# Kernel optimization log

Hardware: AMD Instinct MI355X
Metric: run time of the kernel (lower is better)

## Reference

```python
import math
import jax, jax.numpy as jnp
import numpy as np

N_HEADS = 12


def _rel_to_abs(x):
    # x: [b, h, L, 2L-1] relative logits -> [b, h, L, L] absolute-position scores
    b, h, L, _ = x.shape
    x = jnp.pad(x, ((0, 0), (0, 0), (0, 0), (0, 1)))           # [b,h,L,2L]
    xf = x.reshape(b, h, L * 2 * L)
    xf = jnp.pad(xf, ((0, 0), (0, 0), (0, L - 1)))
    return xf.reshape(b, h, L + 1, 2 * L - 1)[:, :, :L, L - 1:]


def _abs_to_rel(x):
    # x: [b, h, L, L] attention weights -> [b, h, L, 2L-1] relative-position weights
    b, h, L, _ = x.shape
    x = jnp.pad(x, ((0, 0), (0, 0), (0, 0), (0, L - 1)))        # [b,h,L,2L-1]
    xf = x.reshape(b, h, L * (2 * L - 1))
    xf = jnp.pad(xf, ((0, 0), (0, 0), (L, 0)))
    return xf.reshape(b, h, L, 2 * L)[:, :, :, 1:]


def _get_relative_embeddings(emb, length):
    # emb: [n_rel, 2*window+1, k] -> [n_rel, 2*length-1, k]
    window = (emb.shape[1] - 1) // 2
    pad_len = max(length - (window + 1), 0)
    start = max(window + 1 - length, 0)
    if pad_len > 0:
        emb = jnp.pad(emb, ((0, 0), (pad_len, pad_len), (0, 0)))
    return emb[:, start:start + 2 * length - 1]


def setup_inputs() -> dict:
    key = jax.random.key(0)
    ks = jax.random.split(key, 8)
    B, C, T, H = 4, 768, 1024, N_HEADS
    K = C // H
    W = 10
    xavier = math.sqrt(2.0 / (C + C))          # xavier_uniform std analogue
    rel_std = K ** (-0.5)
    return {
        "x": jax.random.normal(ks[0], (B, C, T), jnp.float32),
        "c": jax.random.normal(ks[1], (B, C, T), jnp.float32),
        "Wq": jax.random.normal(ks[2], (C, C), jnp.float32) * xavier,
        "bq": jnp.zeros((C,), jnp.float32),
        "Wk": jax.random.normal(ks[3], (C, C), jnp.float32) * xavier,
        "bk": jnp.zeros((C,), jnp.float32),
        "Wv": jax.random.normal(ks[4], (C, C), jnp.float32) * xavier,
        "bv": jnp.zeros((C,), jnp.float32),
        "Wo": jax.random.normal(ks[5], (C, C), jnp.float32) * xavier,
        "bo": jnp.zeros((C,), jnp.float32),
        "emb_rel_k": jax.random.normal(ks[6], (1, 2 * W + 1, K), jnp.float32) * rel_std,
        "emb_rel_v": jax.random.normal(ks[7], (1, 2 * W + 1, K), jnp.float32) * rel_std,
    }


def reference(x, c, Wq, bq, Wk, bk, Wv, bv, Wo, bo, emb_rel_k, emb_rel_v):
    B, C, T = x.shape
    H = N_HEADS
    K = C // H

    def proj(W_, b_, inp):  # Conv1d(kernel=1) == channel-wise linear
        return jnp.einsum('oi,bit->bot', W_, inp) + b_[None, :, None]

    # [B,C,T] -> [B,H,T,K]
    q = proj(Wq, bq, x).reshape(B, H, K, T).transpose(0, 1, 3, 2)
    k = proj(Wk, bk, c).reshape(B, H, K, T).transpose(0, 1, 3, 2)
    v = proj(Wv, bv, c).reshape(B, H, K, T).transpose(0, 1, 3, 2)

    qs = q * (1.0 / math.sqrt(K))
    scores = jnp.einsum('bhtd,bhsd->bhts', qs, k)               # [B,H,T,T]

    # relative key logits via skewing trick
    rel_k = _get_relative_embeddings(emb_rel_k, T)              # [1,2T-1,K]
    rel_logits = jnp.einsum('bhtd,md->bhtm', qs, rel_k[0])      # [B,H,T,2T-1]
    scores = scores + _rel_to_abs(rel_logits)

    # proximal bias: -log(1 + |i - j|)
    r = jnp.arange(T, dtype=scores.dtype)
    scores = scores - jnp.log1p(jnp.abs(r[None, :] - r[:, None]))[None, None]

    p = jax.nn.softmax(scores, axis=-1)
    out = jnp.einsum('bhts,bhsd->bhtd', p, v)                   # [B,H,T,K]

    # relative value contribution
    rel_v = _get_relative_embeddings(emb_rel_v, T)              # [1,2T-1,K]
    out = out + jnp.einsum('bhtm,md->bhtd', _abs_to_rel(p), rel_v[0])

    out = out.transpose(0, 1, 3, 2).reshape(B, C, T)            # [B,C,T]
    return jnp.einsum('oi,bit->bot', Wo, out) + bo[None, :, None]
```

## Files before the change

kernel.cpp:

```cpp
#include <hip/hip_runtime.h>
#include <hip/hip_bf16.h>

using bf16 = __hip_bfloat16;
typedef __attribute__((ext_vector_type(8))) short short8;
typedef __attribute__((ext_vector_type(4))) float f32x4;

static constexpr int C = 768, T = 1024, H = 12, D = 64;

__device__ __forceinline__ f32x4 mfma16(short8 a, short8 b, f32x4 c){
  return __builtin_amdgcn_mfma_f32_16x16x32_bf16(a, b, c, 0, 0, 0);
}

__device__ __forceinline__ void gload16(const void* g, void* l){
  void* gv = const_cast<void*>(g);
  __builtin_amdgcn_global_load_lds((__attribute__((address_space(1))) void*)gv,
                                   (__attribute__((address_space(3))) void*)l, 16, 0, 0);
}

__device__ __forceinline__ float b2f(short s){
  unsigned u = ((unsigned)(unsigned short)s) << 16;
  return __builtin_bit_cast(float, u);
}

__device__ __forceinline__ int cvtpk(float a, float b){
  int r;
  asm("v_cvt_pk_bf16_f32 %0, %1, %2" : "=v"(r) : "v"(a), "v"(b));
  return r;
}

union PkU { int i[4]; short8 v; };

__global__ __launch_bounds__(256) void cvt4_kernel(const float* __restrict__ a,
                                                   const float* __restrict__ b,
                                                   const float* __restrict__ c_,
                                                   const float* __restrict__ d,
                                                   bf16* oa, bf16* ob, bf16* oc, bf16* od){
  const int m = blockIdx.y;
  const float* in = m==0 ? a : m==1 ? b : m==2 ? c_ : d;
  bf16* out = m==0 ? oa : m==1 ? ob : m==2 ? oc : od;
  int i = (blockIdx.x*256 + threadIdx.x)*4;
  float4 v = *(const float4*)(in + i);
  out[i+0] = (bf16)v.x; out[i+1] = (bf16)v.y;
  out[i+2] = (bf16)v.z; out[i+3] = (bf16)v.w;
}

__global__ __launch_bounds__(256) void transpose_cvt2(const float* __restrict__ xin,
                                                      const float* __restrict__ cin,
                                                      bf16* __restrict__ xo,
                                                      bf16* __restrict__ co){
  __shared__ float tile[64][65];
  const int z = blockIdx.z, b = z & 3, which = z >> 2;
  const float* in = which ? cin : xin;
  bf16* out = which ? co : xo;
  const int t0 = blockIdx.x*64, c0 = blockIdx.y*64;
  const int u = threadIdx.x & 63, r0 = threadIdx.x >> 6;
  const float* ip = in + ((size_t)b*C + c0)*T + t0;
  #pragma unroll
  for (int i = r0; i < 64; i += 4) tile[i][u] = ip[(size_t)i*T + u];
  __syncthreads();
  bf16* op = out + ((size_t)b*T + t0)*C + c0;
  #pragma unroll
  for (int j = r0; j < 64; j += 4) op[(size_t)j*C + u] = (bf16)tile[u][j];
}

__global__ __launch_bounds__(256,3) void gemm_qkv(const bf16* __restrict__ xb,
    const bf16* __restrict__ cb, const bf16* __restrict__ wq, const bf16* __restrict__ wk,
    const bf16* __restrict__ wv, const float* __restrict__ bq, const float* __restrict__ bk,
    const float* __restrict__ bv, bf16* __restrict__ qout, bf16* __restrict__ kout,
    bf16* __restrict__ vout){
  const int tid = threadIdx.x, lane = tid & 63, w = tid >> 6;
  const int wr = w >> 1, wc = w & 1, g = lane >> 4, cl = lane & 15;
  const int bz = blockIdx.y, b = bz & 3, mode = bz >> 2;
  const int lb = blockIdx.x;
  int m0, n0;
  if (mode == 2){ m0 = (lb >> 3)*128; n0 = (lb & 7)*128; }
  else          { m0 = (lb / 6)*128;  n0 = (lb % 6)*128; }
  const bf16* A  = (mode==0) ? xb + (size_t)b*T*C : (mode==1) ? cb + (size_t)b*T*C : wv;
  const bf16* Bp = (mode==2) ? cb + (size_t)b*T*C : (mode==0) ? wq : wk;
  const float* bias = (mode==0) ? bq : (mode==1) ? bk : bv;
  const float scale = (mode==0) ? 0.125f*1.44269504088896f : 1.0f;
  __shared__ bf16 lA[128*64], lB[128*64];
  f32x4 acc[4][4] = {};
  const bf16* Ars = A  + (size_t)m0*768;
  const bf16* Brs = Bp + (size_t)n0*768;
  for (int k0 = 0; k0 < 768; k0 += 64){
    __syncthreads();
    #pragma unroll
    for (int rr = 0; rr < 4; ++rr){
      const int u = rr*256 + tid;
      const int row = u >> 3, cc = u & 7;
      const int src = row*768 + k0 + ((cc ^ (row & 7))*8);
      gload16(Ars + src, &lA[(size_t)u*8]);
      gload16(Brs + src, &lB[(size_t)u*8]);
    }
    __syncthreads();
    #pragma unroll
    for (int kh = 0; kh < 2; ++kh){
      short8 af[4], bfr[4];
      #pragma unroll
      for (int mi = 0; mi < 4; ++mi){
        const int row = wr*64 + mi*16 + cl;
        af[mi] = *(const short8*)&lA[row*64 + (((g + kh*4) ^ (row & 7))*8)];
      }
      #pragma unroll
      for (int ni = 0; ni < 4; ++ni){
        const int row = wc*64 + ni*16 + cl;
        bfr[ni] = *(const short8*)&lB[row*64 + (((g + kh*4) ^ (row & 7))*8)];
      }
      __builtin_amdgcn_s_setprio(1);
      #pragma unroll
      for (int mi = 0; mi < 4; ++mi)
        #pragma unroll
        for (int ni = 0; ni < 4; ++ni)
          acc[mi][ni] = mfma16(af[mi], bfr[ni], acc[mi][ni]);
      __builtin_amdgcn_s_setprio(0);
    }
  }
  #pragma unroll
  for (int mi = 0; mi < 4; ++mi){
    const int mB = m0 + wr*64 + mi*16 + g*4;
    #pragma unroll
    for (int ni = 0; ni < 4; ++ni){
      const int n = n0 + wc*64 + ni*16 + cl;
      #pragma unroll
      for (int r = 0; r < 4; ++r){
        const int m = mB + r;
        float v = acc[mi][ni][r];
        if (mode <= 1){
          v = (v + bias[n]) * scale;
          bf16* outp = mode ? kout : qout;
          outp[(size_t)b*(H*T*D) + (size_t)(n >> 6)*(T*D) + (size_t)m*D + (n & 63)] = (bf16)v;
        } else {
          v += bias[m];
          vout[(size_t)b*(C*T) + (size_t)m*T + n] = (bf16)v;
        }
      }
    }
  }
}

__global__ __launch_bounds__(256,3) void gemm_o(const bf16* __restrict__ wo,
                                                const bf16* __restrict__ attn,
                                                const float* __restrict__ bias,
                                                float* __restrict__ outp){
  const int tid = threadIdx.x, lane = tid & 63, w = tid >> 6;
  const int wr = w >> 1, wc = w & 1, g = lane >> 4, cl = lane & 15;
  const int b = blockIdx.z;
  const int m0 = blockIdx.x*128, n0 = blockIdx.y*128;
  __shared__ bf16 lA[128*64], lB[128*64];
  f32x4 acc[4][4] = {};
  const bf16* Ars = wo + (size_t)m0*768;
  const bf16* Brs = attn + (size_t)b*T*C + (size_t)n0*768;
  for (int k0 = 0; k0 < 768; k0 += 64){
    __syncthreads();
    #pragma unroll
    for (int rr = 0; rr < 4; ++rr){
      const int u = rr*256 + tid;
      const int row = u >> 3, cc = u & 7;
      const int src = row*768 + k0 + ((cc ^ (row & 7))*8);
      gload16(Ars + src, &lA[(size_t)u*8]);
      gload16(Brs + src, &lB[(size_t)u*8]);
    }
    __syncthreads();
    #pragma unroll
    for (int kh = 0; kh < 2; ++kh){
      short8 af[4], bfr[4];
      #pragma unroll
      for (int mi = 0; mi < 4; ++mi){
        const int row = wr*64 + mi*16 + cl;
        af[mi] = *(const short8*)&lA[row*64 + (((g + kh*4) ^ (row & 7))*8)];
      }
      #pragma unroll
      for (int ni = 0; ni < 4; ++ni){
        const int row = wc*64 + ni*16 + cl;
        bfr[ni] = *(const short8*)&lB[row*64 + (((g + kh*4) ^ (row & 7))*8)];
      }
      __builtin_amdgcn_s_setprio(1);
      #pragma unroll
      for (int mi = 0; mi < 4; ++mi)
        #pragma unroll
        for (int ni = 0; ni < 4; ++ni)
          acc[mi][ni] = mfma16(af[mi], bfr[ni], acc[mi][ni]);
      __builtin_amdgcn_s_setprio(0);
    }
  }
  #pragma unroll
  for (int mi = 0; mi < 4; ++mi){
    const int mB = m0 + wr*64 + mi*16 + g*4;
    #pragma unroll
    for (int ni = 0; ni < 4; ++ni){
      const int n = n0 + wc*64 + ni*16 + cl;
      #pragma unroll
      for (int r = 0; r < 4; ++r){
        const int m = mB + r;
        outp[(size_t)b*(C*T) + (size_t)m*T + n] = acc[mi][ni][r] + bias[m];
      }
    }
  }
}

__global__ __launch_bounds__(256,3) void attn_kernel(const bf16* __restrict__ qws,
                                                     const bf16* __restrict__ kws,
                                                     const bf16* __restrict__ vws,
                                                     bf16* __restrict__ aws,
                                                     const float* __restrict__ relk,
                                                     const float* __restrict__ relv){
  const int tid = threadIdx.x, lane = tid & 63, w = tid >> 6;
  const int g = lane >> 4, cl = lane & 15;
  const int i0 = blockIdx.x*64, bh = blockIdx.y;
  const int b = bh / H, h = bh % H;
  const int ql = w*16 + cl;
  const int qt = i0 + ql;

  __shared__ __align__(16) char smem[40960];
  bf16*  lKV   = (bf16*)smem;
  float* bandS = (float*)(smem + 32768);
  bf16*  relkD = (bf16*)(smem + 38144);
  bf16*  lEmb32 = lKV + 4096;
  bf16*  lEV    = lKV;
  bf16*  lQ     = lKV + 3*4096;

  const bf16* qg = qws + ((size_t)bh*T + i0)*D;
  const bf16* kg = kws + (size_t)bh*T*D;
  const bf16* vg = vws + ((size_t)b*C + h*D)*T;

  int kOff[2], vOff[2], qOff[2], dst[2];
  #pragma unroll
  for (int r = 0; r < 2; ++r){
    const int u = r*256 + tid, L = u >> 3, cc = u & 7;
    const int sc8 = (cc ^ (L & 7))*8;
    const int sig = (((L>>4)&1)<<5) | (((L>>2)&3)<<3) | (((L>>5)&1)<<2) | (L&3);
    kOff[r] = sig*64 + sc8;
    vOff[r] = L*T + sc8;
    qOff[r] = L*64 + sc8;
    dst[r]  = u*8;
  }

  #pragma unroll
  for (int r = 0; r < 2; ++r){
    gload16(qg + qOff[r], &lQ[dst[r]]);
    gload16(kg + kOff[r], &lKV[dst[r]]);
    gload16(vg + vOff[r], &lKV[2*4096 + dst[r]]);
  }
  for (int idx = tid; idx < 2048; idx += 256){
    const int row = idx >> 6, col = idx & 63;
    const float v = (row < 21) ? relk[idx] : 0.0f;
    lEmb32[row*64 + (((col >> 3) ^ (row & 7))*8) + (col & 7)] = (bf16)v;
  }
  __syncthreads();

  const short8 aq0 = *(const short8*)&lQ[ql*64 + ((g ^ (ql & 7))*8)];
  const short8 aq1 = *(const short8*)&lQ[ql*64 + (((g + 4) ^ (ql & 7))*8)];

  #pragma unroll
  for (int ni2 = 0; ni2 < 2; ++ni2){
    const int row = ni2*16 + cl;
    short8 e0 = *(const short8*)&lEmb32[row*64 + ((g ^ (row & 7))*8)];
    short8 e1 = *(const short8*)&lEmb32[row*64 + (((g + 4) ^ (row & 7))*8)];
    f32x4 rk = {};
    rk = mfma16(e0, aq0, rk);
    rk = mfma16(e1, aq1, rk);
    #pragma unroll
    for (int rr = 0; rr < 4; ++rr){
      const int ridx = ni2*16 + 4*g + rr;
      if (ridx < 21) relkD[ql*22 + ridx] = (bf16)rk[rr];
    }
  }
  __syncthreads();

  float mreg = -1e30f, lreg = 0.f;
  f32x4 o[4] = {};
  const int koffA[4] = {8*g, 32 + 8*g, 4 + 8*g, 36 + 8*g};

  for (int jt = 0; jt < 16; ++jt){
    const int j0 = jt*64, cur = jt & 1, nxt = cur ^ 1;
    if (jt < 15){
      const int jn = j0 + 64;
      #pragma unroll
      for (int r = 0; r < 2; ++r){
        gload16(kg + jn*64 + kOff[r], &lKV[nxt*4096 + dst[r]]);
        gload16(vg + jn + vOff[r],    &lKV[(2 + nxt)*4096 + dst[r]]);
      }
    }
    const bf16* Kc = lKV + cur*4096;
    const bf16* Vc = lKV + (2 + cur)*4096;

    f32x4 s[4] = {};
    __builtin_amdgcn_s_setprio(1);
    #pragma unroll
    for (int ni = 0; ni < 4; ++ni){
      const int row = ni*16 + cl;
      short8 k0f = *(const short8*)&Kc[row*64 + ((g ^ (row & 7))*8)];
      s[ni] = mfma16(k0f, aq0, s[ni]);
      short8 k1f = *(const short8*)&Kc[row*64 + (((g + 4) ^ (row & 7))*8)];
      s[ni] = mfma16(k1f, aq1, s[ni]);
    }
    __builtin_amdgcn_s_setprio(0);

    const int dj = j0 - i0;
    if (dj == 0 || dj == 64 || dj == -64){
      #pragma unroll
      for (int ni = 0; ni < 4; ++ni){
        const int ibase = j0 + koffA[ni] - qt;
        #pragma unroll
        for (int r = 0; r < 4; ++r){
          const int dd = ibase + r;
          float v = s[ni][r] - __log2f(fabsf((float)dd) + 1.0f);
          if ((unsigned)(dd + 10) <= 20u){
            v += b2f(*(const short*)&relkD[ql*22 + dd + 10]);
            bandS[ql*21 + dd + 10] = v;
          }
          s[ni][r] = v;
        }
      }
    } else {
      #pragma unroll
      for (int ni = 0; ni < 4; ++ni){
        const float fb = (float)(j0 + koffA[ni] - qt);
        #pragma unroll
        for (int r = 0; r < 4; ++r)
          s[ni][r] -= __log2f(fabsf(fb + (float)r) + 1.0f);
      }
    }

    float m0 = fmaxf(fmaxf(s[0][0], s[0][1]), fmaxf(s[0][2], s[0][3]));
    float m1 = fmaxf(fmaxf(s[1][0], s[1][1]), fmaxf(s[1][2], s[1][3]));
    float m2 = fmaxf(fmaxf(s[2][0], s[2][1]), fmaxf(s[2][2], s[2][3]));
    float m3 = fmaxf(fmaxf(s[3][0], s[3][1]), fmaxf(s[3][2], s[3][3]));
    float mx = fmaxf(fmaxf(m0, m1), fmaxf(m2, m3));
    mx = fmaxf(mx, __shfl_xor(mx, 16));
    mx = fmaxf(mx, __shfl_xor(mx, 32));
    const float mn = fmaxf(mreg, mx);
    if (!__all(mn == mreg)){
      const float sc = __builtin_amdgcn_exp2f(mreg - mn);
      lreg *= sc;
      #pragma unroll
      for (int di = 0; di < 4; ++di)
        #pragma unroll
        for (int r = 0; r < 4; ++r) o[di][r] *= sc;
      mreg = mn;
    }
    float rs = 0.f;
    #pragma unroll
    for (int ni = 0; ni < 4; ++ni)
      #pragma unroll
      for (int r = 0; r < 4; ++r){
        float p = __builtin_amdgcn_exp2f(s[ni][r] - mreg);
        s[ni][r] = p; rs += p;
      }
    rs += __shfl_xor(rs, 16);
    rs += __shfl_xor(rs, 32);
    lreg += rs;

    PkU bf0, bf1;
    bf0.i[0] = cvtpk(s[0][0], s[0][1]); bf0.i[1] = cvtpk(s[0][2], s[0][3]);
    bf0.i[2] = cvtpk(s[2][0], s[2][1]); bf0.i[3] = cvtpk(s[2][2], s[2][3]);
    bf1.i[0] = cvtpk(s[1][0], s[1][1]); bf1.i[1] = cvtpk(s[1][2], s[1][3]);
    bf1.i[2] = cvtpk(s[3][0], s[3][1]); bf1.i[3] = cvtpk(s[3][2], s[3][3]);

    __builtin_amdgcn_s_setprio(1);
    #pragma unroll
    for (int di = 0; di < 4; ++di){
      const int vrow = di*16 + cl;
      short8 a0 = *(const short8*)&Vc[vrow*64 + ((g ^ (vrow & 7))*8)];
      o[di] = mfma16(a0, bf0.v, o[di]);
      short8 a1 = *(const short8*)&Vc[vrow*64 + (((g + 4) ^ (vrow & 7))*8)];
      o[di] = mfma16(a1, bf1.v, o[di]);
    }
    __builtin_amdgcn_s_setprio(0);
    __syncthreads();
  }

  for (int idx = tid; idx < 2048; idx += 256){
    const int d = idx >> 5, c = idx & 31;
    const float v = (c < 21) ? relv[c*64 + d] : 0.0f;
    lEV[d*32 + (((c >> 3) ^ ((d >> 2) & 3))*8) + (c & 7)] = (bf16)v;
  }
  __syncthreads();

  const float invl = 1.0f / lreg;
  float pb[8];
  #pragma unroll
  for (int e = 0; e < 8; ++e){
    const int ddi = 8*g + e;
    float pv = 0.f;
    if (ddi < 21){
      const int j = qt + ddi - 10;
      if (j >= 0 && j < T)
        pv = __builtin_amdgcn_exp2f(bandS[ql*21 + ddi] - mreg) * invl;
    }
    pb[e] = pv;
  }
  PkU bfE;
  bfE.i[0] = cvtpk(pb[0], pb[1]); bfE.i[1] = cvtpk(pb[2], pb[3]);
  bfE.i[2] = cvtpk(pb[4], pb[5]); bfE.i[3] = cvtpk(pb[6], pb[7]);

  bf16* outp = aws + (size_t)(b*T + qt)*C + h*64;
  #pragma unroll
  for (int di = 0; di < 4; ++di){
    const int arow = di*16 + cl;
    short8 aE = *(const short8*)&lEV[arow*32 + ((g ^ ((arow >> 2) & 3))*8)];
    f32x4 z = {};
    f32x4 ba = mfma16(aE, bfE.v, z);
    const int p0 = cvtpk(o[di][0]*invl + ba[0], o[di][1]*invl + ba[1]);
    const int p1 = cvtpk(o[di][2]*invl + ba[2], o[di][3]*invl + ba[3]);
    *(int2*)(outp + di*16 + 4*g) = make_int2(p0, p1);
  }
}

extern "C" void kernel_launch(void* const* d_in, const int* in_sizes, int n_in,
                              void* d_out, int out_size, void* d_ws, size_t ws_size,
                              hipStream_t stream){
  const float* x    = (const float*)d_in[0];
  const float* cin  = (const float*)d_in[1];
  const float* Wq   = (const float*)d_in[2];
  const float* bq   = (const float*)d_in[3];
  const float* Wk   = (const float*)d_in[4];
  const float* bk   = (const float*)d_in[5];
  const float* Wv   = (const float*)d_in[6];
  const float* bv   = (const float*)d_in[7];
  const float* Wo   = (const float*)d_in[8];
  const float* bo   = (const float*)d_in[9];
  const float* relk = (const float*)d_in[10];
  const float* relv = (const float*)d_in[11];

  char* ws = (char*)d_ws;
  constexpr size_t SZ_W = (size_t)768*768*2;
  constexpr size_t SZ_T = (size_t)4*1024*768*2;
  bf16* wq  = (bf16*)(ws + 0*SZ_W);
  bf16* wk  = (bf16*)(ws + 1*SZ_W);
  bf16* wv  = (bf16*)(ws + 2*SZ_W);
  bf16* wo  = (bf16*)(ws + 3*SZ_W);
  bf16* xb  = (bf16*)(ws + 4*SZ_W);
  bf16* cb  = (bf16*)(ws + 4*SZ_W + 1*SZ_T);
  bf16* qws = (bf16*)(ws + 4*SZ_W + 2*SZ_T);
  bf16* kws = (bf16*)(ws + 4*SZ_W + 3*SZ_T);
  bf16* vws = (bf16*)(ws + 4*SZ_W + 4*SZ_T);
  bf16* attn = xb;

  cvt4_kernel<<<dim3(576,4), 256, 0, stream>>>(Wq, Wk, Wv, Wo, wq, wk, wv, wo);
  transpose_cvt2<<<dim3(16,12,8), 256, 0, stream>>>(x, cin, xb, cb);
  gemm_qkv<<<dim3(48,12), 256, 0, stream>>>(xb, cb, wq, wk, wv, bq, bk, bv, qws, kws, vws);
  attn_kernel<<<dim3(16,48), 256, 0, stream>>>(qws, kws, vws, attn, relk, relv);
  gemm_o<<<dim3(6,8,4), 256, 0, stream>>>(wo, attn, bo, (float*)d_out);
}
```

Measured before the change: 100.7 us.

## Merge prep kernels, load V fragments directly to registers in attention

```diff
diff --git a/kernel.cpp b/kernel.cpp
--- a/kernel.cpp
+++ b/kernel.cpp
@@ -30,37 +30,37 @@
 
 union PkU { int i[4]; short8 v; };
 
-__global__ __launch_bounds__(256) void cvt4_kernel(const float* __restrict__ a,
-                                                   const float* __restrict__ b,
-                                                   const float* __restrict__ c_,
-                                                   const float* __restrict__ d,
-                                                   bf16* oa, bf16* ob, bf16* oc, bf16* od){
-  const int m = blockIdx.y;
-  const float* in = m==0 ? a : m==1 ? b : m==2 ? c_ : d;
-  bf16* out = m==0 ? oa : m==1 ? ob : m==2 ? oc : od;
-  int i = (blockIdx.x*256 + threadIdx.x)*4;
-  float4 v = *(const float4*)(in + i);
-  out[i+0] = (bf16)v.x; out[i+1] = (bf16)v.y;
-  out[i+2] = (bf16)v.z; out[i+3] = (bf16)v.w;
-}
-
-__global__ __launch_bounds__(256) void transpose_cvt2(const float* __restrict__ xin,
-                                                      const float* __restrict__ cin,
-                                                      bf16* __restrict__ xo,
-                                                      bf16* __restrict__ co){
-  __shared__ float tile[64][65];
-  const int z = blockIdx.z, b = z & 3, which = z >> 2;
-  const float* in = which ? cin : xin;
-  bf16* out = which ? co : xo;
-  const int t0 = blockIdx.x*64, c0 = blockIdx.y*64;
-  const int u = threadIdx.x & 63, r0 = threadIdx.x >> 6;
-  const float* ip = in + ((size_t)b*C + c0)*T + t0;
-  #pragma unroll
-  for (int i = r0; i < 64; i += 4) tile[i][u] = ip[(size_t)i*T + u];
-  __syncthreads();
-  bf16* op = out + ((size_t)b*T + t0)*C + c0;
-  #pragma unroll
-  for (int j = r0; j < 64; j += 4) op[(size_t)j*C + u] = (bf16)tile[u][j];
+__global__ __launch_bounds__(256) void prep_kernel(const float* __restrict__ xin,
+    const float* __restrict__ cin, const float* __restrict__ Wq,
+    const float* __restrict__ Wk, const float* __restrict__ Wv,
+    const float* __restrict__ Wo, bf16* __restrict__ xo, bf16* __restrict__ co,
+    bf16* __restrict__ wq, bf16* __restrict__ wk, bf16* __restrict__ wv,
+    bf16* __restrict__ wo){
+  const int z = blockIdx.z;
+  if (z < 8){
+    __shared__ float tile[64][65];
+    const int b = z & 3, which = z >> 2;
+    const float* in = which ? cin : xin;
+    bf16* out = which ? co : xo;
+    const int t0 = blockIdx.x*64, c0 = blockIdx.y*64;
+    const int u = threadIdx.x & 63, r0 = threadIdx.x >> 6;
+    const float* ip = in + ((size_t)b*C + c0)*T + t0;
+    #pragma unroll
+    for (int i = r0; i < 64; i += 4) tile[i][u] = ip[(size_t)i*T + u];
+    __syncthreads();
+    bf16* op = out + ((size_t)b*T + t0)*C + c0;
+    #pragma unroll
+    for (int j = r0; j < 64; j += 4) op[(size_t)j*C + u] = (bf16)tile[u][j];
+  } else {
+    const int chunk = (z - 8)*192 + blockIdx.y*16 + blockIdx.x;
+    const int m = chunk / 576;
+    const int off = (chunk % 576)*1024 + threadIdx.x*4;
+    const float* in = m==0 ? Wq : m==1 ? Wk : m==2 ? Wv : Wo;
+    bf16* out = m==0 ? wq : m==1 ? wk : m==2 ? wv : wo;
+    float4 v = *(const float4*)(in + off);
+    out[off+0] = (bf16)v.x; out[off+1] = (bf16)v.y;
+    out[off+2] = (bf16)v.z; out[off+3] = (bf16)v.w;
+  }
 }
 
 __global__ __launch_bounds__(256,3) void gemm_qkv(const bf16* __restrict__ xb,
@@ -199,7 +199,7 @@
   }
 }
 
-__global__ __launch_bounds__(256,3) void attn_kernel(const bf16* __restrict__ qws,
+__global__ __launch_bounds__(256,5) void attn_kernel(const bf16* __restrict__ qws,
                                                      const bf16* __restrict__ kws,
                                                      const bf16* __restrict__ vws,
                                                      bf16* __restrict__ aws,
@@ -212,26 +212,25 @@
   const int ql = w*16 + cl;
   const int qt = i0 + ql;
 
-  __shared__ __align__(16) char smem[40960];
-  bf16*  lKV   = (bf16*)smem;
-  float* bandS = (float*)(smem + 32768);
-  bf16*  relkD = (bf16*)(smem + 38144);
-  bf16*  lEmb32 = lKV + 4096;
-  bf16*  lEV    = lKV;
-  bf16*  lQ     = lKV + 3*4096;
+  __shared__ __align__(16) char smem[24576];
+  bf16*  lK     = (bf16*)smem;
+  float* bandS  = (float*)(smem + 16384);
+  bf16*  relkD  = (bf16*)(smem + 21760);
+  bf16*  lEmb32 = (bf16*)(smem + 16384);
+  bf16*  lEV    = (bf16*)smem;
+  bf16*  lQ     = lK + 4096;
 
   const bf16* qg = qws + ((size_t)bh*T + i0)*D;
   const bf16* kg = kws + (size_t)bh*T*D;
   const bf16* vg = vws + ((size_t)b*C + h*D)*T;
 
-  int kOff[2], vOff[2], qOff[2], dst[2];
+  int kOff[2], qOff[2], dst[2];
   #pragma unroll
   for (int r = 0; r < 2; ++r){
     const int u = r*256 + tid, L = u >> 3, cc = u & 7;
     const int sc8 = (cc ^ (L & 7))*8;
     const int sig = (((L>>4)&1)<<5) | (((L>>2)&3)<<3) | (((L>>5)&1)<<2) | (L&3);
     kOff[r] = sig*64 + sc8;
-    vOff[r] = L*T + sc8;
     qOff[r] = L*64 + sc8;
     dst[r]  = u*8;
   }
@@ -239,8 +238,7 @@
   #pragma unroll
   for (int r = 0; r < 2; ++r){
     gload16(qg + qOff[r], &lQ[dst[r]]);
-    gload16(kg + kOff[r], &lKV[dst[r]]);
-    gload16(vg + vOff[r], &lKV[2*4096 + dst[r]]);
+    gload16(kg + kOff[r], &lK[dst[r]]);
   }
   for (int idx = tid; idx < 2048; idx += 256){
     const int row = idx >> 6, col = idx & 63;
@@ -274,16 +272,22 @@
 
   for (int jt = 0; jt < 16; ++jt){
     const int j0 = jt*64, cur = jt & 1, nxt = cur ^ 1;
+
+    short8 va[8];
+    #pragma unroll
+    for (int di = 0; di < 4; ++di){
+      const bf16* p = vg + (size_t)(di*16 + cl)*T + j0 + 8*g;
+      va[di*2 + 0] = *(const short8*)(p);
+      va[di*2 + 1] = *(const short8*)(p + 32);
+    }
+
     if (jt < 15){
       const int jn = j0 + 64;
       #pragma unroll
-      for (int r = 0; r < 2; ++r){
-        gload16(kg + jn*64 + kOff[r], &lKV[nxt*4096 + dst[r]]);
-        gload16(vg + jn + vOff[r],    &lKV[(2 + nxt)*4096 + dst[r]]);
-      }
-    }
-    const bf16* Kc = lKV + cur*4096;
-    const bf16* Vc = lKV + (2 + cur)*4096;
+      for (int r = 0; r < 2; ++r)
+        gload16(kg + jn*64 + kOff[r], &lK[nxt*4096 + dst[r]]);
+    }
+    const bf16* Kc = lK + cur*4096;
 
     f32x4 s[4] = {};
     __builtin_amdgcn_s_setprio(1);
@@ -361,11 +365,8 @@
     __builtin_amdgcn_s_setprio(1);
     #pragma unroll
     for (int di = 0; di < 4; ++di){
-      const int vrow = di*16 + cl;
-      short8 a0 = *(const short8*)&Vc[vrow*64 + ((g ^ (vrow & 7))*8)];
-      o[di] = mfma16(a0, bf0.v, o[di]);
-      short8 a1 = *(const short8*)&Vc[vrow*64 + (((g + 4) ^ (vrow & 7))*8)];
-      o[di] = mfma16(a1, bf1.v, o[di]);
+      o[di] = mfma16(va[di*2 + 0], bf0.v, o[di]);
+      o[di] = mfma16(va[di*2 + 1], bf1.v, o[di]);
     }
     __builtin_amdgcn_s_setprio(0);
     __syncthreads();
@@ -438,8 +439,8 @@
   bf16* vws = (bf16*)(ws + 4*SZ_W + 4*SZ_T);
   bf16* attn = xb;
 
-  cvt4_kernel<<<dim3(576,4), 256, 0, stream>>>(Wq, Wk, Wv, Wo, wq, wk, wv, wo);
-  transpose_cvt2<<<dim3(16,12,8), 256, 0, stream>>>(x, cin, xb, cb);
+  prep_kernel<<<dim3(16,12,20), 256, 0, stream>>>(x, cin, Wq, Wk, Wv, Wo,
+                                                  xb, cb, wq, wk, wv, wo);
   gemm_qkv<<<dim3(48,12), 256, 0, stream>>>(xb, cb, wq, wk, wv, bq, bk, bv, qws, kws, vws);
   attn_kernel<<<dim3(16,48), 256, 0, stream>>>(qws, kws, vws, attn, relk, relv);
   gemm_o<<<dim3(6,8,4), 256, 0, stream>>>(wo, attn, bo, (float*)d_out);
```

Measured after the change: 163.3 us. 62.1% more time.
